# Optimization experiments

Measured on AMD Instinct MI355X. Metric: run time of the kernel, lower is better.

## Reference

```python
import jax, jax.numpy as jnp
import numpy as np

PAD = 0  # padding_index
BIG = 10000.0

B, S = 1024, 128
V, E, H, T = 200, 512, 512, 24


def setup_inputs() -> dict:
    key = jax.random.key(0)
    ks = jax.random.split(key, 12)
    sequences = jax.random.randint(ks[0], (B, S), 0, V, dtype=jnp.int32)
    labels = jax.random.randint(ks[1], (B, S), 0, T, dtype=jnp.int32)
    true_lengths = jax.random.randint(ks[2], (B,), 1, S, dtype=jnp.int32)
    emb = jax.random.normal(ks[3], (V, E), dtype=jnp.float32) * 0.1
    emb = emb.at[PAD].set(0.0)  # nn.Embedding padding_idx zeros that row
    w1 = jax.random.normal(ks[4], (H, H), dtype=jnp.float32) * (1.0 / np.sqrt(H))
    b1 = jax.random.normal(ks[5], (H,), dtype=jnp.float32) * 0.01
    w2 = jax.random.normal(ks[6], (T, H), dtype=jnp.float32) * (1.0 / np.sqrt(H))
    b2 = jax.random.normal(ks[7], (T,), dtype=jnp.float32) * 0.01
    start_trans = jax.random.uniform(ks[8], (T,), jnp.float32, -0.1, 0.1)
    end_trans = jax.random.uniform(ks[9], (T,), jnp.float32, -0.1, 0.1)
    transitions = jax.random.uniform(ks[10], (T, T), jnp.float32, -0.1, 0.1)
    return {"sequences": sequences, "labels": labels, "true_lengths": true_lengths,
            "emb": emb, "w1": w1, "b1": b1, "w2": w2, "b2": b2,
            "start_trans": start_trans, "end_trans": end_trans, "transitions": transitions}


def _emissions(sequences, emb, w1, b1, w2, b2):
    pad_mask = (sequences == PAD).astype(jnp.float32)  # [B,S]
    x = emb[sequences]                                  # [B,S,E]
    h = jax.nn.relu(x @ w1.T + b1)                      # [B,S,H]
    scores = jax.nn.relu(h @ w2.T + b2)                 # [B,S,T]
    scores = scores.at[:, :, PAD].add(pad_mask * BIG)
    return scores


def _crf_nll_mean(emissions, labels, start_trans, end_trans, transitions):
    # emissions [B,S,T], labels [B,S]; mask = all ones (none passed in forward)
    # numerator: score of gold path
    em_gold = jnp.take_along_axis(emissions, labels[..., None], axis=2)[..., 0]  # [B,S]
    num = (start_trans[labels[:, 0]]
           + em_gold.sum(axis=1)
           + transitions[labels[:, :-1], labels[:, 1:]].sum(axis=1)
           + end_trans[labels[:, -1]])  # [B]
    # denominator: forward algorithm via scan over time
    em_t = jnp.swapaxes(emissions, 0, 1)  # [S,B,T]
    alpha0 = start_trans[None, :] + em_t[0]  # [B,T]

    def step(alpha, emit):
        # alpha [B,T_prev], transitions [T_prev,T_next], emit [B,T_next]
        nxt = jax.nn.logsumexp(alpha[:, :, None] + transitions[None] + emit[:, None, :], axis=1)
        return nxt, None

    alpha, _ = jax.lax.scan(step, alpha0, em_t[1:])
    denom = jax.nn.logsumexp(alpha + end_trans[None, :], axis=1)  # [B]
    llh = num - denom
    return -jnp.mean(llh)


def reference(sequences, labels, true_lengths, emb, w1, b1, w2, b2,
              start_trans, end_trans, transitions):
    emissions = _emissions(sequences, emb, w1, b1, w2, b2)
    return _crf_nll_mean(emissions, labels, start_trans, end_trans, transitions)
```

## Files before the change

kernel.cpp:

```cpp
#include <hip/hip_runtime.h>
#include <math.h>

#define PAD_IDX 0
#define BIGV 10000.0f
constexpr int B_ = 1024, S_ = 128, V_ = 200, E_ = 512, H_ = 512, T_ = 24;

constexpr int OFF_H  = 262144;
constexpr int OFF_EM = 364544;
constexpr int OFF_W  = 369344;
constexpr int OFF_MX = 374144;

__device__ __forceinline__ unsigned short f2bf(float f) {
    unsigned u = __float_as_uint(f);
    u += 0x7fffu + ((u >> 16) & 1u);
    return (unsigned short)(u >> 16);
}

__global__ __launch_bounds__(256) void transpose_kernel(
    const float* __restrict__ w1, unsigned short* __restrict__ w1Tb,
    float* __restrict__ out)
{
    __shared__ float tile[64][65];
    const int bi = blockIdx.x >> 3, bj = blockIdx.x & 7;
    const int tx = threadIdx.x & 63, r0 = (threadIdx.x >> 6) * 16;
    if (blockIdx.x == 0 && threadIdx.x == 0) out[0] = 0.f;
    #pragma unroll
    for (int m = 0; m < 16; ++m) {
        const int r = r0 + m;
        tile[r][tx] = w1[(size_t)(bi * 64 + r) * 512 + bj * 64 + tx];
    }
    __syncthreads();
    #pragma unroll
    for (int m = 0; m < 16; ++m) {
        const int r = r0 + m;
        w1Tb[(size_t)(bj * 64 + r) * 512 + bi * 64 + tx] = f2bf(tile[tx][r]);
    }
}

__global__ __launch_bounds__(256) void h_kernel(
    const float* __restrict__ emb, const unsigned short* __restrict__ w1Tb,
    const float* __restrict__ b1, float* __restrict__ h_ws)
{
    __shared__ float xi[2 * E_];
    __shared__ float part_s[4][64][8];
    const int pair = blockIdx.x >> 1, half = blockIdx.x & 1;
    const int v0 = pair * 2, v1 = v0 + 1;
    const int tid = threadIdx.x;

    {
        const float* __restrict__ x0 = emb + (size_t)v0 * E_;
        const float* __restrict__ x1 = emb + (size_t)v1 * E_;
        #pragma unroll
        for (int m = 0; m < 2; ++m) {
            const int k = tid + m * 256;
            xi[2 * k]     = x0[k];
            xi[2 * k + 1] = x1[k];
        }
    }
    __syncthreads();

    const int part = tid >> 6;
    const int quad = tid & 63;
    const int t0 = half * 256 + quad * 4;
    const int k0 = part * 128;

    float a0 = 0.f, a1 = 0.f, a2 = 0.f, a3 = 0.f;
    float c0 = 0.f, c1 = 0.f, c2 = 0.f, c3 = 0.f;
    const unsigned short* __restrict__ wp = w1Tb + (size_t)k0 * H_ + t0;
    const float2* __restrict__ xp = (const float2*)xi + k0;
    #pragma unroll 4
    for (int i = 0; i < 128; ++i) {
        const uint2 wu = *(const uint2*)(wp + (size_t)i * H_);
        const float2 x = xp[i];
        const float w0 = __uint_as_float(wu.x << 16);
        const float w1v = __uint_as_float(wu.x & 0xffff0000u);
        const float w2v = __uint_as_float(wu.y << 16);
        const float w3v = __uint_as_float(wu.y & 0xffff0000u);
        a0 = fmaf(w0,  x.x, a0); a1 = fmaf(w1v, x.x, a1);
        a2 = fmaf(w2v, x.x, a2); a3 = fmaf(w3v, x.x, a3);
        c0 = fmaf(w0,  x.y, c0); c1 = fmaf(w1v, x.y, c1);
        c2 = fmaf(w2v, x.y, c2); c3 = fmaf(w3v, x.y, c3);
    }
    part_s[part][quad][0] = a0; part_s[part][quad][1] = a1;
    part_s[part][quad][2] = a2; part_s[part][quad][3] = a3;
    part_s[part][quad][4] = c0; part_s[part][quad][5] = c1;
    part_s[part][quad][6] = c2; part_s[part][quad][7] = c3;
    __syncthreads();

    {
        const int q2 = tid >> 2, r0 = tid & 3;
        const float s0 = (part_s[0][q2][r0]     + part_s[1][q2][r0])
                       + (part_s[2][q2][r0]     + part_s[3][q2][r0]);
        const float s1 = (part_s[0][q2][r0 + 4] + part_s[1][q2][r0 + 4])
                       + (part_s[2][q2][r0 + 4] + part_s[3][q2][r0 + 4]);
        const int t = half * 256 + tid;
        const float bb = b1[t];
        h_ws[(size_t)v0 * H_ + t] = fmaxf(s0 + bb, 0.f);
        h_ws[(size_t)v1 * H_ + t] = fmaxf(s1 + bb, 0.f);
    }
}

__global__ __launch_bounds__(256) void emis_kernel(
    const float* __restrict__ h_ws, const float* __restrict__ w2,
    const float* __restrict__ b2, float* __restrict__ em_table,
    float* __restrict__ w_table, float* __restrict__ emax_arr)
{
    __shared__ float em_row[32];
    const int v = blockIdx.x;
    const int t = threadIdx.x;
    const int wave = t >> 6, lane = t & 63;
    const float* __restrict__ hrow = h_ws + (size_t)v * H_;

    for (int jj2 = 0; jj2 < 6; ++jj2) {
        const int jo = wave * 6 + jj2;
        float part = 0.f;
        #pragma unroll
        for (int m = 0; m < H_ / 64; ++m) {
            const int k = lane + m * 64;
            part = fmaf(hrow[k], w2[(size_t)jo * H_ + k], part);
        }
        #pragma unroll
        for (int off = 32; off; off >>= 1)
            part += __shfl_xor(part, off, 64);
        if (lane == 0) {
            float val = fmaxf(part + b2[jo], 0.f);
            if (v == 0 && jo == PAD_IDX) val += BIGV;
            em_row[jo] = val;
        }
    }
    __syncthreads();

    if (t < 32) {
        float x = (t < T_) ? em_row[t] : -INFINITY;
        float mx = x;
        #pragma unroll
        for (int off = 16; off; off >>= 1)
            mx = fmaxf(mx, __shfl_xor(mx, off, 32));
        if (t < T_) {
            em_table[v * T_ + t] = x;
            w_table[v * T_ + t]  = __expf(x - mx);
        }
        if (t == 0) emax_arr[v] = mx;
    }
}

#define BC(q, i) __uint_as_float(__builtin_amdgcn_ds_swizzle((q), (i) << 5))
#define ACC4U(base)                                      \
    s0 = fmaf(BC(qi, (base)),     Ecoef[(base)],     s0); \
    s1 = fmaf(BC(qi, (base) + 1), Ecoef[(base) + 1], s1); \
    s2 = fmaf(BC(qi, (base) + 2), Ecoef[(base) + 2], s2); \
    s3 = fmaf(BC(qi, (base) + 3), Ecoef[(base) + 3], s3);

__global__ __launch_bounds__(256) void crf_kernel(
    const int* __restrict__ seq, const int* __restrict__ labels,
    const float* __restrict__ start_t, const float* __restrict__ end_t,
    const float* __restrict__ trans, const float* __restrict__ em_table,
    const float* __restrict__ w_table, const float* __restrict__ emax_arr,
    float* __restrict__ out)
{
    __shared__ __align__(16) float w_s[V_ * T_];
    __shared__ float emax_s[V_];
    __shared__ int   tok_s[4 * S_];
    const int tid = threadIdx.x;
    {
        const float4* __restrict__ src = (const float4*)w_table;
        float4* dst = (float4*)w_s;
        for (int i = tid; i < V_ * T_ / 4; i += 256) dst[i] = src[i];
    }
    for (int i = tid; i < V_; i += 256) emax_s[i] = emax_arr[i];
    {
        const int base = blockIdx.x * 4 * S_;
        #pragma unroll
        for (int i = 0; i < 2; ++i)
            tok_s[tid + i * 256] = seq[base + tid + i * 256];
    }
    __syncthreads();

    const int wave = tid >> 6, lane = tid & 63;
    const int b = blockIdx.x * 4 + wave;
    const int jl = lane & 31;
    const int jj = (jl < T_) ? jl : 0;
    const bool act = (jl < T_);
    const bool isF = (lane < 32);
    const int* __restrict__ lrow = labels + (size_t)b * S_;
    const int* __restrict__ tks  = tok_s + wave * S_;

    float Ecoef[T_];
    #pragma unroll
    for (int i = 0; i < T_; ++i) {
        const int tix = isF ? (i * T_ + jj) : (jj * T_ + i);
        Ecoef[i] = act ? __expf(trans[tix]) : 0.f;
    }

    const int tokI = isF ? tks[0] : tks[S_ - 1];
    const float bse = isF ? start_t[jj] : end_t[jj];
    const float a0v = bse + em_table[tokI * T_ + jj];
    float m0 = act ? a0v : -INFINITY;
    #pragma unroll
    for (int off = 16; off; off >>= 1)
        m0 = fmaxf(m0, __shfl_xor(m0, off, 32));
    const float qFi = __expf(a0v - m0);
    const float qBi = w_s[tokI * T_ + jj] * __expf(bse);
    float q = act ? (isF ? qFi : qBi) : 0.f;
    float logacc = isF ? m0 : 0.f;

    const int dir_l = isF ? 1 : -1;
    const int off_l = isF ? 0 : 127;

    float wv = w_s[tks[off_l + dir_l] * T_ + jj];
    int tokN = tks[off_l + dir_l * 2];

    for (int s = 1; s <= 63; ++s) {
        const float wn = w_s[tokN * T_ + jj];
        const int nxt = (s + 2 <= 63) ? s + 2 : 63;
        const int tokC = tks[off_l + dir_l * nxt];
        const unsigned qi = __float_as_uint(q);
        float s0 = 0.f, s1 = 0.f, s2 = 0.f, s3 = 0.f;
        ACC4U(0) ACC4U(4) ACC4U(8) ACC4U(12) ACC4U(16) ACC4U(20)
        q = ((s0 + s1) + (s2 + s3)) * wv;
        wv = wn; tokN = tokC;
        if ((s & 15) == 0) {
            float m = q;
            #pragma unroll
            for (int off = 16; off; off >>= 1)
                m = fmaxf(m, __shfl_xor(m, off, 32));
            q *= (1.0f / m);
            logacc += __logf(m);
        }
    }

    {
        float m = q;
        #pragma unroll
        for (int off = 16; off; off >>= 1)
            m = fmaxf(m, __shfl_xor(m, off, 32));
        q *= (1.0f / m);
        logacc += __logf(m);
    }

    float u;
    {
        const unsigned qi = __float_as_uint(q);
        float s0 = 0.f, s1 = 0.f, s2 = 0.f, s3 = 0.f;
        ACC4U(0) ACC4U(4) ACC4U(8) ACC4U(12) ACC4U(16) ACC4U(20)
        u = (s0 + s1) + (s2 + s3);
    }

    const float sel = isF ? u : q;
    const float oth = __shfl_xor(sel, 32, 64);
    float prod = sel * oth;
    #pragma unroll
    for (int off = 32; off; off >>= 1)
        prod += __shfl_xor(prod, off, 64);
    const float logacc_o = __shfl_xor(logacc, 32, 64);
    const float denom = logacc + logacc_o + __logf(0.5f * prod);

    float gp = 0.f;
    #pragma unroll
    for (int r = 0; r < 2; ++r) {
        const int s = lane + r * 64;
        const int tk = tks[s];
        const int ls = lrow[s];
        gp += em_table[tk * T_ + ls];
        if (s >= 1) gp -= emax_s[tk];
        if (s < S_ - 1) gp += trans[ls * T_ + lrow[s + 1]];
        if (s == 0) gp += start_t[ls];
        if (s == S_ - 1) gp += end_t[ls];
    }
    #pragma unroll
    for (int off = 32; off; off >>= 1)
        gp += __shfl_xor(gp, off, 64);

    if (lane == 0)
        atomicAdd(out, (denom - gp) * (1.0f / (float)B_));
}

extern "C" void kernel_launch(void* const* d_in, const int* in_sizes, int n_in,
                              void* d_out, int out_size, void* d_ws, size_t ws_size,
                              hipStream_t stream) {
    const int*   seq     = (const int*)d_in[0];
    const int*   labels  = (const int*)d_in[1];
    const float* emb     = (const float*)d_in[3];
    const float* w1      = (const float*)d_in[4];
    const float* b1      = (const float*)d_in[5];
    const float* w2      = (const float*)d_in[6];
    const float* b2      = (const float*)d_in[7];
    const float* start_t = (const float*)d_in[8];
    const float* end_t   = (const float*)d_in[9];
    const float* trans   = (const float*)d_in[10];

    float* ws       = (float*)d_ws;
    unsigned short* w1Tb = (unsigned short*)d_ws;
    float* h_ws     = ws + OFF_H;
    float* em_table = ws + OFF_EM;
    float* w_table  = ws + OFF_W;
    float* emax_arr = ws + OFF_MX;
    float* out      = (float*)d_out;

    transpose_kernel<<<64, 256, 0, stream>>>(w1, w1Tb, out);
    h_kernel<<<200, 256, 0, stream>>>(emb, w1Tb, b1, h_ws);
    emis_kernel<<<V_, 256, 0, stream>>>(h_ws, w2, b2, em_table, w_table, emax_arr);
    crf_kernel<<<B_ / 4, 256, 0, stream>>>(seq, labels, start_t, end_t, trans,
                                           em_table, w_table, emax_arr, out);
}
```

Measured before the change: 121.2 us.

## Batch CRF forward recursion over 32 sequences with bf16 MFMA

The CRF forward/backward recursion now processes 32 sequences per block as a 32x32x16 bf16 MFMA matrix product at each time step, where before one wave handled one sequence with ds_swizzle broadcast FMAs. Alpha vectors are repacked to bf16 each step and exchanged between wave halves with shuffles. The gold-path score moves into its own small kernel. The aim is to replace the per-sequence scalar recurrence with matrix-core throughput, at the cost of bf16 rounding in the recurrence, one extra launch, and only 32 blocks of 2 waves.

```diff
diff --git a/kernel.cpp b/kernel.cpp
--- a/kernel.cpp
+++ b/kernel.cpp
@@ -9,11 +9,20 @@
 constexpr int OFF_EM = 364544;
 constexpr int OFF_W  = 369344;
 constexpr int OFF_MX = 374144;
+constexpr int OFF_GP = 374344;
+
+typedef __attribute__((ext_vector_type(8)))  short    bf8frag;
+typedef __attribute__((ext_vector_type(16))) float    facc16;
+typedef __attribute__((ext_vector_type(4)))  unsigned u32x4;
 
 __device__ __forceinline__ unsigned short f2bf(float f) {
     unsigned u = __float_as_uint(f);
     u += 0x7fffu + ((u >> 16) & 1u);
     return (unsigned short)(u >> 16);
+}
+__device__ __forceinline__ unsigned pkbf(float lo, float hi) {
+    const unsigned a = __float_as_uint(lo), b = __float_as_uint(hi);
+    return ((a + 0x8000u) >> 16) | ((b + 0x8000u) & 0xffff0000u);
 }
 
 __global__ __launch_bounds__(256) void transpose_kernel(
@@ -46,7 +55,6 @@
     const int pair = blockIdx.x >> 1, half = blockIdx.x & 1;
     const int v0 = pair * 2, v1 = v0 + 1;
     const int tid = threadIdx.x;
-
     {
         const float* __restrict__ x0 = emb + (size_t)v0 * E_;
         const float* __restrict__ x1 = emb + (size_t)v1 * E_;
@@ -58,12 +66,8 @@
         }
     }
     __syncthreads();
-
-    const int part = tid >> 6;
-    const int quad = tid & 63;
-    const int t0 = half * 256 + quad * 4;
-    const int k0 = part * 128;
-
+    const int part = tid >> 6, quad = tid & 63;
+    const int t0 = half * 256 + quad * 4, k0 = part * 128;
     float a0 = 0.f, a1 = 0.f, a2 = 0.f, a3 = 0.f;
     float c0 = 0.f, c1 = 0.f, c2 = 0.f, c3 = 0.f;
     const unsigned short* __restrict__ wp = w1Tb + (size_t)k0 * H_ + t0;
@@ -86,7 +90,6 @@
     part_s[part][quad][4] = c0; part_s[part][quad][5] = c1;
     part_s[part][quad][6] = c2; part_s[part][quad][7] = c3;
     __syncthreads();
-
     {
         const int q2 = tid >> 2, r0 = tid & 3;
         const float s0 = (part_s[0][q2][r0]     + part_s[1][q2][r0])
@@ -110,7 +113,6 @@
     const int t = threadIdx.x;
     const int wave = t >> 6, lane = t & 63;
     const float* __restrict__ hrow = h_ws + (size_t)v * H_;
-
     for (int jj2 = 0; jj2 < 6; ++jj2) {
         const int jo = wave * 6 + jj2;
         float part = 0.f;
@@ -129,7 +131,6 @@
         }
     }
     __syncthreads();
-
     if (t < 32) {
         float x = (t < T_) ? em_row[t] : -INFINITY;
         float mx = x;
@@ -144,135 +145,226 @@
     }
 }
 
-#define BC(q, i) __uint_as_float(__builtin_amdgcn_ds_swizzle((q), (i) << 5))
-#define ACC4U(base)                                      \
-    s0 = fmaf(BC(qi, (base)),     Ecoef[(base)],     s0); \
-    s1 = fmaf(BC(qi, (base) + 1), Ecoef[(base) + 1], s1); \
-    s2 = fmaf(BC(qi, (base) + 2), Ecoef[(base) + 2], s2); \
-    s3 = fmaf(BC(qi, (base) + 3), Ecoef[(base) + 3], s3);
-
-__global__ __launch_bounds__(256) void crf_kernel(
+__global__ __launch_bounds__(256) void gold_kernel(
     const int* __restrict__ seq, const int* __restrict__ labels,
     const float* __restrict__ start_t, const float* __restrict__ end_t,
     const float* __restrict__ trans, const float* __restrict__ em_table,
-    const float* __restrict__ w_table, const float* __restrict__ emax_arr,
+    const float* __restrict__ emax_arr, float* __restrict__ gp_ws)
+{
+    const int grp = threadIdx.x >> 5, j = threadIdx.x & 31;
+    const int b = blockIdx.x * 8 + grp;
+    const int* __restrict__ srow = seq + (size_t)b * S_;
+    const int* __restrict__ lrow = labels + (size_t)b * S_;
+    float gp = 0.f;
+    #pragma unroll
+    for (int r = 0; r < 4; ++r) {
+        const int s = j + r * 32;
+        const int tk = srow[s], ls = lrow[s];
+        gp += em_table[tk * T_ + ls];
+        if (s >= 1) gp -= emax_arr[tk];
+        if (s < S_ - 1) gp += trans[ls * T_ + lrow[s + 1]];
+        if (s == 0) gp += start_t[ls];
+        if (s == S_ - 1) gp += end_t[ls];
+    }
+    #pragma unroll
+    for (int off = 16; off; off >>= 1)
+        gp += __shfl_xor(gp, off, 32);
+    if (j == 0) gp_ws[b] = gp;
+}
+
+__global__ __launch_bounds__(128) void crf_kernel(
+    const int* __restrict__ seq,
+    const float* __restrict__ start_t, const float* __restrict__ end_t,
+    const float* __restrict__ trans, const float* __restrict__ em_table,
+    const float* __restrict__ w_table, const float* __restrict__ gp_ws,
     float* __restrict__ out)
 {
     __shared__ __align__(16) float w_s[V_ * T_];
-    __shared__ float emax_s[V_];
-    __shared__ int   tok_s[4 * S_];
+    __shared__ int   tok_s[S_ * 32];
+    __shared__ float meet_s[64 * 12];
+    __shared__ float logb_s[64];
     const int tid = threadIdx.x;
-    {
-        const float4* __restrict__ src = (const float4*)w_table;
-        float4* dst = (float4*)w_s;
-        for (int i = tid; i < V_ * T_ / 4; i += 256) dst[i] = src[i];
-    }
-    for (int i = tid; i < V_; i += 256) emax_s[i] = emax_arr[i];
-    {
-        const int base = blockIdx.x * 4 * S_;
-        #pragma unroll
-        for (int i = 0; i < 2; ++i)
-            tok_s[tid + i * 256] = seq[base + tid + i * 256];
-    }
-    __syncthreads();
-
-    const int wave = tid >> 6, lane = tid & 63;
-    const int b = blockIdx.x * 4 + wave;
-    const int jl = lane & 31;
-    const int jj = (jl < T_) ? jl : 0;
-    const bool act = (jl < T_);
-    const bool isF = (lane < 32);
-    const int* __restrict__ lrow = labels + (size_t)b * S_;
-    const int* __restrict__ tks  = tok_s + wave * S_;
-
-    float Ecoef[T_];
-    #pragma unroll
-    for (int i = 0; i < T_; ++i) {
-        const int tix = isF ? (i * T_ + jj) : (jj * T_ + i);
-        Ecoef[i] = act ? __expf(trans[tix]) : 0.f;
-    }
-
-    const int tokI = isF ? tks[0] : tks[S_ - 1];
-    const float bse = isF ? start_t[jj] : end_t[jj];
-    const float a0v = bse + em_table[tokI * T_ + jj];
-    float m0 = act ? a0v : -INFINITY;
-    #pragma unroll
-    for (int off = 16; off; off >>= 1)
-        m0 = fmaxf(m0, __shfl_xor(m0, off, 32));
-    const float qFi = __expf(a0v - m0);
-    const float qBi = w_s[tokI * T_ + jj] * __expf(bse);
-    float q = act ? (isF ? qFi : qBi) : 0.f;
-    float logacc = isF ? m0 : 0.f;
-
-    const int dir_l = isF ? 1 : -1;
-    const int off_l = isF ? 0 : 127;
-
-    float wv = w_s[tks[off_l + dir_l] * T_ + jj];
-    int tokN = tks[off_l + dir_l * 2];
-
+    const int g = blockIdx.x;
+
+    for (int i = tid; i < V_ * T_ / 4; i += 128)
+        ((float4*)w_s)[i] = ((const float4*)w_table)[i];
+    {
+        const int bq = tid & 31, c = tid >> 5;
+        const int* __restrict__ src = seq + (size_t)(g * 32 + bq) * S_ + c * 32;
+        #pragma unroll 4
+        for (int i = 0; i < 32; ++i)
+            tok_s[(c * 32 + i) * 32 + bq] = src[i];
+    }
+    __syncthreads();
+
+    const bool isF = (tid < 64);
+    const int lane = tid & 63;
+    const int n = lane & 31;
+    const int h = lane >> 5;
+
+    u32x4 A1p, A2p;
+    {
+        float a1e[8], a2e[8];
+        #pragma unroll
+        for (int j = 0; j < 8; ++j) {
+            const int k1 = 8 * h + j;
+            const int k2 = 16 + 8 * h + j;
+            float v1 = 0.f, v2 = 0.f;
+            if (n < T_) {
+                v1 = __expf(isF ? trans[k1 * T_ + n] : trans[n * T_ + k1]);
+                if (k2 < T_)
+                    v2 = __expf(isF ? trans[k2 * T_ + n] : trans[n * T_ + k2]);
+            }
+            a1e[j] = v1; a2e[j] = v2;
+        }
+        #pragma unroll
+        for (int r = 0; r < 4; ++r) {
+            A1p[r] = pkbf(a1e[2 * r], a1e[2 * r + 1]);
+            A2p[r] = pkbf(a2e[2 * r], a2e[2 * r + 1]);
+        }
+    }
+
+    float logacc;
+    u32x4 B1p, B2p;
+    {
+        const int tokI = tok_s[(isF ? 0 : (S_ - 1)) * 32 + n];
+        float q1[8], q2[8];
+        if (isF) {
+            float e1[8], e2[8];
+            #pragma unroll
+            for (int j = 0; j < 8; ++j) { e1[j] = 0.f; e2[j] = 0.f; }
+            float mx = -INFINITY;
+            #pragma unroll
+            for (int j = 0; j < 8; ++j) {
+                const int r1 = 8 * h + j;
+                e1[j] = start_t[r1] + em_table[tokI * T_ + r1];
+                mx = fmaxf(mx, e1[j]);
+            }
+            if (h == 0) {
+                #pragma unroll
+                for (int j = 0; j < 8; ++j) {
+                    const int r2 = 16 + j;
+                    e2[j] = start_t[r2] + em_table[tokI * T_ + r2];
+                    mx = fmaxf(mx, e2[j]);
+                }
+            }
+            mx = fmaxf(mx, __shfl_xor(mx, 32, 64));
+            #pragma unroll
+            for (int j = 0; j < 8; ++j) {
+                q1[j] = __expf(e1[j] - mx);
+                q2[j] = (h == 0) ? __expf(e2[j] - mx) : 0.f;
+            }
+            logacc = mx;
+        } else {
+            #pragma unroll
+            for (int j = 0; j < 8; ++j) {
+                const int r1 = 8 * h + j;
+                q1[j] = w_s[tokI * T_ + r1] * __expf(end_t[r1]);
+                const int r2 = 16 + j;
+                q2[j] = (h == 0) ? w_s[tokI * T_ + r2] * __expf(end_t[r2]) : 0.f;
+            }
+            logacc = 0.f;
+        }
+        #pragma unroll
+        for (int r = 0; r < 4; ++r) {
+            B1p[r] = pkbf(q1[2 * r], q1[2 * r + 1]);
+            B2p[r] = pkbf(q2[2 * r], q2[2 * r + 1]);
+        }
+    }
+
+    const int dir  = isF ? 1 : -1;
+    const int offi = isF ? 1 : (S_ - 2);
+
+    float4 Wc0, Wc1, Wc2;
+    {
+        const int tk = tok_s[offi * 32 + n];
+        const float* wb = w_s + tk * T_ + 4 * h;
+        Wc0 = *(const float4*)(wb);
+        Wc1 = *(const float4*)(wb + 8);
+        Wc2 = *(const float4*)(wb + 16);
+    }
+
+    float d[12];
     for (int s = 1; s <= 63; ++s) {
-        const float wn = w_s[tokN * T_ + jj];
-        const int nxt = (s + 2 <= 63) ? s + 2 : 63;
-        const int tokC = tks[off_l + dir_l * nxt];
-        const unsigned qi = __float_as_uint(q);
-        float s0 = 0.f, s1 = 0.f, s2 = 0.f, s3 = 0.f;
-        ACC4U(0) ACC4U(4) ACC4U(8) ACC4U(12) ACC4U(16) ACC4U(20)
-        q = ((s0 + s1) + (s2 + s3)) * wv;
-        wv = wn; tokN = tokC;
-        if ((s & 15) == 0) {
-            float m = q;
-            #pragma unroll
-            for (int off = 16; off; off >>= 1)
-                m = fmaxf(m, __shfl_xor(m, off, 32));
-            q *= (1.0f / m);
-            logacc += __logf(m);
-        }
-    }
-
-    {
-        float m = q;
-        #pragma unroll
-        for (int off = 16; off; off >>= 1)
-            m = fmaxf(m, __shfl_xor(m, off, 32));
-        q *= (1.0f / m);
-        logacc += __logf(m);
-    }
-
-    float u;
-    {
-        const unsigned qi = __float_as_uint(q);
-        float s0 = 0.f, s1 = 0.f, s2 = 0.f, s3 = 0.f;
-        ACC4U(0) ACC4U(4) ACC4U(8) ACC4U(12) ACC4U(16) ACC4U(20)
-        u = (s0 + s1) + (s2 + s3);
-    }
-
-    const float sel = isF ? u : q;
-    const float oth = __shfl_xor(sel, 32, 64);
-    float prod = sel * oth;
-    #pragma unroll
-    for (int off = 32; off; off >>= 1)
-        prod += __shfl_xor(prod, off, 64);
-    const float logacc_o = __shfl_xor(logacc, 32, 64);
-    const float denom = logacc + logacc_o + __logf(0.5f * prod);
-
-    float gp = 0.f;
-    #pragma unroll
-    for (int r = 0; r < 2; ++r) {
-        const int s = lane + r * 64;
-        const int tk = tks[s];
-        const int ls = lrow[s];
-        gp += em_table[tk * T_ + ls];
-        if (s >= 1) gp -= emax_s[tk];
-        if (s < S_ - 1) gp += trans[ls * T_ + lrow[s + 1]];
-        if (s == 0) gp += start_t[ls];
-        if (s == S_ - 1) gp += end_t[ls];
-    }
-    #pragma unroll
-    for (int off = 32; off; off >>= 1)
-        gp += __shfl_xor(gp, off, 64);
-
-    if (lane == 0)
-        atomicAdd(out, (denom - gp) * (1.0f / (float)B_));
+        const int sn = (s < 63) ? (s + 1) : 63;
+        const int tkN = tok_s[(offi + dir * (sn - 1)) * 32 + n];
+        const float* wbn = w_s + tkN * T_ + 4 * h;
+        const float4 Wn0 = *(const float4*)(wbn);
+        const float4 Wn1 = *(const float4*)(wbn + 8);
+        const float4 Wn2 = *(const float4*)(wbn + 16);
+
+        facc16 acc;
+        #pragma unroll
+        for (int r = 0; r < 16; ++r) acc[r] = 0.f;
+        acc = __builtin_amdgcn_mfma_f32_32x32x16_bf16(
+                  __builtin_bit_cast(bf8frag, A2p),
+                  __builtin_bit_cast(bf8frag, B2p), acc, 0, 0, 0);
+        acc = __builtin_amdgcn_mfma_f32_32x32x16_bf16(
+                  __builtin_bit_cast(bf8frag, A1p),
+                  __builtin_bit_cast(bf8frag, B1p), acc, 0, 0, 0);
+
+        d[0] = acc[0]*Wc0.x;  d[1] = acc[1]*Wc0.y;  d[2]  = acc[2]*Wc0.z;  d[3]  = acc[3]*Wc0.w;
+        d[4] = acc[4]*Wc1.x;  d[5] = acc[5]*Wc1.y;  d[6]  = acc[6]*Wc1.z;  d[7]  = acc[7]*Wc1.w;
+        d[8] = acc[8]*Wc2.x;  d[9] = acc[9]*Wc2.y;  d[10] = acc[10]*Wc2.z; d[11] = acc[11]*Wc2.w;
+
+        if ((s & 15) == 0 || s == 63) {
+            float mx = d[0];
+            #pragma unroll
+            for (int r = 1; r < 12; ++r) mx = fmaxf(mx, d[r]);
+            mx = fmaxf(mx, __shfl_xor(mx, 32, 64));
+            const float inv = 1.0f / mx;
+            #pragma unroll
+            for (int r = 0; r < 12; ++r) d[r] *= inv;
+            logacc += __logf(mx);
+        }
+
+        const unsigned P0 = pkbf(d[0], d[1]),  P1 = pkbf(d[2], d[3]);
+        const unsigned P2 = pkbf(d[4], d[5]),  P3 = pkbf(d[6], d[7]);
+        const unsigned P4 = pkbf(d[8], d[9]),  P5 = pkbf(d[10], d[11]);
+        const unsigned XP0 = (unsigned)__shfl_xor((int)P0, 32, 64);
+        const unsigned XP1 = (unsigned)__shfl_xor((int)P1, 32, 64);
+        const unsigned XP2 = (unsigned)__shfl_xor((int)P2, 32, 64);
+        const unsigned XP3 = (unsigned)__shfl_xor((int)P3, 32, 64);
+        const unsigned XP4 = (unsigned)__shfl_xor((int)P4, 32, 64);
+        const unsigned XP5 = (unsigned)__shfl_xor((int)P5, 32, 64);
+        B1p[0] = h ? XP2 : P0;  B1p[1] = h ? XP3 : P1;
+        B1p[2] = h ? P2  : XP0; B1p[3] = h ? P3  : XP1;
+        B2p[0] = h ? 0u  : P4;  B2p[1] = h ? 0u  : P5;
+        B2p[2] = h ? 0u  : XP4; B2p[3] = h ? 0u  : XP5;
+
+        Wc0 = Wn0; Wc1 = Wn1; Wc2 = Wn2;
+    }
+
+    if (!isF) {
+        #pragma unroll
+        for (int r = 0; r < 12; ++r) meet_s[lane * 12 + r] = d[r];
+        logb_s[lane] = logacc;
+    }
+    __syncthreads();
+    if (isF) {
+        facc16 acc;
+        #pragma unroll
+        for (int r = 0; r < 16; ++r) acc[r] = 0.f;
+        acc = __builtin_amdgcn_mfma_f32_32x32x16_bf16(
+                  __builtin_bit_cast(bf8frag, A2p),
+                  __builtin_bit_cast(bf8frag, B2p), acc, 0, 0, 0);
+        acc = __builtin_amdgcn_mfma_f32_32x32x16_bf16(
+                  __builtin_bit_cast(bf8frag, A1p),
+                  __builtin_bit_cast(bf8frag, B1p), acc, 0, 0, 0);
+        float dot = 0.f;
+        #pragma unroll
+        for (int r = 0; r < 12; ++r)
+            dot = fmaf(acc[r], meet_s[lane * 12 + r], dot);
+        dot += __shfl_xor(dot, 32, 64);
+        const float denom = logacc + logb_s[lane] + __logf(dot);
+        float val = 0.f;
+        if (h == 0)
+            val = (denom - gp_ws[g * 32 + n]) * (1.0f / (float)B_);
+        #pragma unroll
+        for (int off = 32; off; off >>= 1)
+            val += __shfl_xor(val, off, 64);
+        if (lane == 0) atomicAdd(out, val);
+    }
 }
 
 extern "C" void kernel_launch(void* const* d_in, const int* in_sizes, int n_in,
@@ -295,11 +387,14 @@
     float* em_table = ws + OFF_EM;
     float* w_table  = ws + OFF_W;
     float* emax_arr = ws + OFF_MX;
+    float* gp_ws    = ws + OFF_GP;
     float* out      = (float*)d_out;
 
     transpose_kernel<<<64, 256, 0, stream>>>(w1, w1Tb, out);
     h_kernel<<<200, 256, 0, stream>>>(emb, w1Tb, b1, h_ws);
     emis_kernel<<<V_, 256, 0, stream>>>(h_ws, w2, b2, em_table, w_table, emax_arr);
-    crf_kernel<<<B_ / 4, 256, 0, stream>>>(seq, labels, start_t, end_t, trans,
-                                           em_table, w_table, emax_arr, out);
-}
+    gold_kernel<<<B_ / 8, 256, 0, stream>>>(seq, labels, start_t, end_t, trans,
+                                            em_table, emax_arr, gp_ws);
+    crf_kernel<<<B_ / 32, 128, 0, stream>>>(seq, start_t, end_t, trans,
+                                            em_table, w_table, gp_ws, out);
+}
```

After: 119.6 us. About the same (-1.3%).
